# Kernel optimization log

Measured on AMD Instinct MI355X. Metric: run time of the kernel, lower is better.

Reference implementation:

```python
import jax, jax.numpy as jnp
import numpy as np

DN = ('NHWC', 'HWIO', 'NHWC')

def _conv1x1(x, k):
    # 1x1 conv, stride 1, SAME padding (channels_last)
    return jax.lax.conv_general_dilated(x, k, window_strides=(1, 1), padding='SAME', dimension_numbers=DN)

def setup_inputs() -> dict:
    key = jax.random.key(0)
    k1, k2, k3, k4, k5 = jax.random.split(key, 5)
    B, H, W, C = 4, 64, 64, 256
    c8 = C // 8
    x = jax.random.normal(k1, (B, H, W, C), dtype=jnp.float32)
    # Glorot-like scaling for stability
    kernel_f = jax.random.normal(k2, (1, 1, C, c8), dtype=jnp.float32) * (1.0 / np.sqrt(C))
    kernel_g = jax.random.normal(k3, (1, 1, C, c8), dtype=jnp.float32) * (1.0 / np.sqrt(C))
    kernel_h = jax.random.normal(k4, (1, 1, C, C), dtype=jnp.float32) * (1.0 / np.sqrt(C))
    gamma = jax.random.normal(k5, (), dtype=jnp.float32) * 0.1
    return {'x': x, 'kernel_f': kernel_f, 'kernel_g': kernel_g, 'kernel_h': kernel_h, 'gamma': gamma}

def reference(x, kernel_f, kernel_g, kernel_h, gamma):
    B, H, W, C = x.shape
    N = H * W
    f = _conv1x1(x, kernel_f).reshape(B, N, -1)   # [B, N, C/8] queries
    g = _conv1x1(x, kernel_g).reshape(B, N, -1)   # [B, N, C/8] keys
    h = _conv1x1(x, kernel_h).reshape(B, N, -1)   # [B, N, C]   values
    e = jnp.einsum('bnc,bmc->bnm', f, g)          # [B, N, N] scores
    attn = jax.nn.softmax(e, axis=-1)
    o = jnp.einsum('bnm,bmc->bnc', attn, h).reshape(B, H, W, C)
    return x + gamma * o
```

## Files before the change

### kernel.cpp

```cpp
#include <hip/hip_runtime.h>

typedef __attribute__((ext_vector_type(8))) short bf16x8;
typedef __attribute__((ext_vector_type(4))) float f32x4;
typedef __attribute__((ext_vector_type(16))) float f32x16;

__device__ __forceinline__ unsigned short f2bf(float f) {
    union { float f; unsigned u; } v; v.f = f;
    return (unsigned short)((v.u + 0x7FFFu + ((v.u >> 16) & 1u)) >> 16);
}

__device__ __forceinline__ float fexp2(float v) {
#if __has_builtin(__builtin_amdgcn_exp2f)
    return __builtin_amdgcn_exp2f(v);
#else
    float r; asm("v_exp_f32 %0, %1" : "=v"(r) : "v"(v)); return r;
#endif
}
__device__ __forceinline__ unsigned cvt_pk_bf16(float lo, float hi) {
    unsigned r;
    asm("v_cvt_pk_bf16_f32 %0, %1, %2" : "=v"(r) : "v"(lo), "v"(hi));
    return r;
}

__device__ __forceinline__ void async16(unsigned short* lds, const unsigned short* gsrc) {
    __builtin_amdgcn_global_load_lds(
        (const __attribute__((address_space(1))) void*)gsrc,
        (__attribute__((address_space(3))) void*)lds, 16, 0, 0);
}

__global__ __launch_bounds__(256) void k_wt(const float* __restrict__ kf,
                                            const float* __restrict__ kg,
                                            const float* __restrict__ kh,
                                            unsigned short* __restrict__ wt) {
    int n = blockIdx.x, t = threadIdx.x;
    const float* src; int stride, col;
    if (n < 32)      { src = kf; stride = 32;  col = n; }
    else if (n < 64) { src = kg; stride = 32;  col = n - 32; }
    else             { src = kh; stride = 256; col = n - 64; }
    float v = src[t * stride + col];
    if (n < 32) v *= 1.44269504088896341f;
    wt[n * 256 + (((t >> 3) ^ (n & 7)) << 3) + (t & 7)] = f2bf(v);
}

__global__ __launch_bounds__(512) void k_proj(const float* __restrict__ x,
                                              const unsigned short* __restrict__ wt,
                                              unsigned short* __restrict__ f,
                                              unsigned short* __restrict__ g,
                                              unsigned short* __restrict__ hT) {
    __shared__ unsigned short xs[8192];
    __shared__ unsigned short ws[16384];
    int t = threadIdx.x, rb = blockIdx.x;
    int w = t >> 6, lane = t & 63, q = lane >> 4, n15 = lane & 15;
    int b = rb >> 7, nbase = (rb & 127) * 32;
    int rg0 = w & 1, cg0 = w >> 1;
    int cgh = w & 3, rgh = w >> 2;

#pragma unroll
    for (int i = 0; i < 4; ++i) {
        int lin = i * 512 + t, row = lin >> 6, c4 = lin & 63;
        float4 v = *(const float4*)&x[(rb * 32 + row) * 256 + c4 * 4];
        ushort4 o; o.x = f2bf(v.x); o.y = f2bf(v.y); o.z = f2bf(v.z); o.w = f2bf(v.w);
        *(ushort4*)&xs[row * 256 + (((c4 >> 1) ^ (row & 7)) << 3) + ((c4 & 1) << 2)] = o;
    }
#pragma unroll
    for (int j = 0; j < 4; ++j)
        async16(&ws[(j * 512 + w * 64) * 8], wt + (j * 512 + t) * 8);
    __syncthreads();

    for (int ct = 0; ct < 5; ++ct) {
        f32x4 acc = (f32x4){0.f, 0.f, 0.f, 0.f};
        if (ct == 0) {
#pragma unroll
            for (int kk = 0; kk < 8; ++kk) {
                bf16x8 a = *(const bf16x8*)&xs[(rg0 * 16 + n15) * 256
                                + ((((kk << 2) + q) ^ (n15 & 7)) << 3)];
                bf16x8 bw = *(const bf16x8*)&ws[(cg0 * 16 + n15) * 256
                                + ((((kk << 2) + q) ^ (n15 & 7)) << 3)];
                acc = __builtin_amdgcn_mfma_f32_16x16x32_bf16(a, bw, acc, 0, 0, 0);
            }
        } else {
#pragma unroll
            for (int kk = 0; kk < 8; ++kk) {
                bf16x8 a = *(const bf16x8*)&ws[(cgh * 16 + n15) * 256
                                + ((((kk << 2) + q) ^ (n15 & 7)) << 3)];
                bf16x8 bx = *(const bf16x8*)&xs[(rgh * 16 + n15) * 256
                                + ((((kk << 2) + q) ^ (n15 & 7)) << 3)];
                acc = __builtin_amdgcn_mfma_f32_16x16x32_bf16(a, bx, acc, 0, 0, 0);
            }
        }
        __syncthreads();
        if (ct < 4) {
            const unsigned short* wsrc = wt + (ct + 1) * 16384;
#pragma unroll
            for (int j = 0; j < 4; ++j)
                async16(&ws[(j * 512 + w * 64) * 8], wsrc + (j * 512 + t) * 8);
        }
        if (ct == 0) {
#pragma unroll
            for (int r = 0; r < 4; ++r) {
                int grow = rb * 32 + rg0 * 16 + q * 4 + r;
                int col = cg0 * 16 + n15;
                unsigned short v = f2bf(acc[r]);
                if (col < 32) f[grow * 32 + col] = v;
                else          g[grow * 32 + (col - 32)] = v;
            }
        } else {
#pragma unroll
            for (int r = 0; r < 4; ++r) {
                int ch = (ct - 1) * 64 + cgh * 16 + q * 4 + r;
                int key = nbase + rgh * 16 + n15;
                hT[((b * 512 + (key >> 3)) * 256 + ch) * 8 + (key & 7)] = f2bf(acc[r]);
            }
        }
        __syncthreads();
    }
}

__global__ __launch_bounds__(512, 4) void k_attn(const float* __restrict__ x,
                                                 const unsigned short* __restrict__ f,
                                                 const unsigned short* __restrict__ g,
                                                 const unsigned short* __restrict__ hT,
                                                 const float* __restrict__ gamma_p,
                                                 float* __restrict__ out) {
    __shared__ unsigned short pls[2][4096];
    __shared__ float lpart[4][64];
    __shared__ __align__(16) float lrec[64];
    int t = threadIdx.x, bx = blockIdx.x;
    int b = (bx >> 1) & 3;
    int ch2 = (bx >> 3) & 1;
    int qt = ((bx & 1) << 5) | (bx >> 4);
    int qbase = qt * 64;
    int chbase = ch2 * 128;
    int w = t >> 6, l = t & 63;
    int hi = l >> 5, l31 = l & 31;
    int q = l >> 4, n15 = l & 15;
    int cb = w & 3;
    const bool is_s = (w < 4);

    bf16x8 aFB[4];
    const unsigned short* gW = g + (b * 4096 + w * 16 + n15) * 32 + q * 8;
    if (is_s) {
#pragma unroll
        for (int nt = 0; nt < 4; ++nt)
            aFB[nt] = *(const bf16x8*)&f[(b * 4096 + qbase + nt * 16 + n15) * 32 + q * 8];
    }
    bf16x8 aG, aGn;
    f32x4 lac = (f32x4){0.f, 0.f, 0.f, 0.f};
    const f32x4 zero4 = (f32x4){0.f, 0.f, 0.f, 0.f};

    const unsigned short* hb2 = hT + b * 1048576
                              + (chbase + cb * 32 + l31) * 8 + hi * 2048;
    bf16x8 bHc[4], bHn[4];

    auto s_tile = [&](int buf) {
        f32x4 sa[4];
#pragma unroll
        for (int nt = 0; nt < 4; ++nt)
            sa[nt] = __builtin_amdgcn_mfma_f32_16x16x32_bf16(aG, aFB[nt], zero4, 0, 0, 0);
        int kq = w * 4 + q;
#pragma unroll
        for (int nt = 0; nt < 4; ++nt) {
#pragma unroll
            for (int r = 0; r < 4; ++r) {
                sa[nt][r] = fexp2(sa[nt][r]);
                lac[nt] += sa[nt][r];
            }
            unsigned p0 = cvt_pk_bf16(sa[nt][0], sa[nt][1]);
            unsigned p1 = cvt_pk_bf16(sa[nt][2], sa[nt][3]);
            int row = nt * 16 + n15;
            unsigned* dst = (unsigned*)&pls[buf][row * 64]
                          + (((kq >> 1) ^ (n15 & 7)) << 2) + ((kq & 1) << 1);
            dst[0] = p0; dst[1] = p1;
        }
    };

    f32x16 o0, o1;
#pragma unroll
    for (int i = 0; i < 16; ++i) { o0[i] = 0.f; o1[i] = 0.f; }

    if (is_s) {
        aG  = *(const bf16x8*)&gW[0];
        aGn = *(const bf16x8*)&gW[2048];
        s_tile(0);
        aG = aGn;
        __builtin_amdgcn_sched_barrier(0);
        asm volatile("s_waitcnt lgkmcnt(0)" ::: "memory");
    } else {
#pragma unroll
        for (int ks = 0; ks < 4; ++ks)
            bHc[ks] = *(const bf16x8*)&hb2[ks * 4096];
        __builtin_amdgcn_sched_barrier(0);
    }
    __builtin_amdgcn_s_barrier();
    __builtin_amdgcn_sched_barrier(0);

#pragma unroll 2
    for (int kt = 0; kt < 64; ++kt) {
        int cur = kt & 1, nxt = cur ^ 1;

        if (is_s) {
            if (kt + 1 < 64) {
                int ktn = (kt + 2 < 64) ? kt + 2 : 63;
                aGn = *(const bf16x8*)&gW[ktn * 2048];
                s_tile(nxt);
                aG = aGn;
            }
            __builtin_amdgcn_sched_barrier(0);
            asm volatile("s_waitcnt lgkmcnt(0)" ::: "memory");
        } else {
            if (kt + 1 < 64) {
#pragma unroll
                for (int ks = 0; ks < 4; ++ks)
                    bHn[ks] = *(const bf16x8*)&hb2[(kt + 1) * 16384 + ks * 4096];
            }
            const unsigned short* pcur = &pls[cur][0];
            __builtin_amdgcn_s_setprio(1);
#pragma unroll
            for (int ks = 0; ks < 4; ++ks) {
                int seg = (((2 * ks + hi) ^ (l31 & 7)) << 3);
                bf16x8 aP0 = *(const bf16x8*)&pcur[l31 * 64 + seg];
                bf16x8 aP1 = *(const bf16x8*)&pcur[(32 + l31) * 64 + seg];
                o0 = __builtin_amdgcn_mfma_f32_32x32x16_bf16(aP0, bHc[ks], o0, 0, 0, 0);
                o1 = __builtin_amdgcn_mfma_f32_32x32x16_bf16(aP1, bHc[ks], o1, 0, 0, 0);
            }
            __builtin_amdgcn_s_setprio(0);
            if (kt + 1 < 64) {
#pragma unroll
                for (int ks = 0; ks < 4; ++ks) bHc[ks] = bHn[ks];
            }
            __builtin_amdgcn_sched_barrier(0);
        }

        __builtin_amdgcn_s_barrier();
        __builtin_amdgcn_sched_barrier(0);
    }

    if (is_s) {
#pragma unroll
        for (int nt = 0; nt < 4; ++nt) {
            float ps = lac[nt];
            ps += __shfl_xor(ps, 16);
            ps += __shfl_xor(ps, 32);
            if (q == 0) lpart[w][nt * 16 + n15] = ps;
        }
    }
    __syncthreads();
    if (t < 64) lrec[t] = 1.0f / (lpart[0][t] + lpart[1][t] + lpart[2][t] + lpart[3][t]);
    __syncthreads();
    if (!is_s) {
        float gam = *gamma_p;
        int ch = chbase + cb * 32 + l31;
#pragma unroll
        for (int qq = 0; qq < 4; ++qq) {
            int r0 = 8 * qq + 4 * hi;
            f32x4 ri0 = *(const f32x4*)&lrec[r0];
            f32x4 ri1 = *(const f32x4*)&lrec[32 + r0];
#pragma unroll
            for (int j = 0; j < 4; ++j) {
                int idx0 = (b * 4096 + qbase + r0 + j) * 256 + ch;
                int idx1 = idx0 + 32 * 256;
                out[idx0] = x[idx0] + gam * (o0[4 * qq + j] * ri0[j]);
                out[idx1] = x[idx1] + gam * (o1[4 * qq + j] * ri1[j]);
            }
        }
    }
}

extern "C" void kernel_launch(void* const* d_in, const int* in_sizes, int n_in,
                              void* d_out, int out_size, void* d_ws, size_t ws_size,
                              hipStream_t stream) {
    const float* x  = (const float*)d_in[0];
    const float* kf = (const float*)d_in[1];
    const float* kg = (const float*)d_in[2];
    const float* kh = (const float*)d_in[3];
    const float* gm = (const float*)d_in[4];
    float* out = (float*)d_out;

    char* ws = (char*)d_ws;
    unsigned short* wt = (unsigned short*)(ws);
    unsigned short* fb = (unsigned short*)(ws + 163840);
    unsigned short* gb = (unsigned short*)(ws + 1212416);
    unsigned short* hT = (unsigned short*)(ws + 2260992);

    hipLaunchKernelGGL(k_wt,   dim3(320), dim3(256), 0, stream, kf, kg, kh, wt);
    hipLaunchKernelGGL(k_proj, dim3(512), dim3(512), 0, stream, x, wt, fb, gb, hT);
    hipLaunchKernelGGL(k_attn, dim3(512), dim3(512), 0, stream, x, fb, gb, hT, gm, out);
}
```

Baseline: 136.6 us.

## Process two key tiles per barrier with quad-buffered P in LDS

The attention main loop now handles two 64-key tiles per iteration, using four LDS buffers for the exponentiated score tile P instead of two. This halves the number of block-wide barriers. Score warps issue two independent MFMA groups back to back, and PV warps run two tiles of MFMAs per phase with register double-buffered H loads. The cost is more LDS per block, which may lower occupancy under launch_bounds(512,4), and more registers.

Result: no change. 138.9 us (+1.7%).

```diff
diff --git a/kernel.cpp b/kernel.cpp
--- a/kernel.cpp
+++ b/kernel.cpp
@@ -122,7 +122,7 @@
                                                  const unsigned short* __restrict__ hT,
                                                  const float* __restrict__ gamma_p,
                                                  float* __restrict__ out) {
-    __shared__ unsigned short pls[2][4096];
+    __shared__ unsigned short pls[4][4096];
     __shared__ float lpart[4][64];
     __shared__ __align__(16) float lrec[64];
     int t = threadIdx.x, bx = blockIdx.x;
@@ -144,7 +144,6 @@
         for (int nt = 0; nt < 4; ++nt)
             aFB[nt] = *(const bf16x8*)&f[(b * 4096 + qbase + nt * 16 + n15) * 32 + q * 8];
     }
-    bf16x8 aG, aGn;
     f32x4 lac = (f32x4){0.f, 0.f, 0.f, 0.f};
     const f32x4 zero4 = (f32x4){0.f, 0.f, 0.f, 0.f};
 
@@ -152,11 +151,12 @@
                               + (chbase + cb * 32 + l31) * 8 + hi * 2048;
     bf16x8 bHc[4], bHn[4];
 
-    auto s_tile = [&](int buf) {
-        f32x4 sa[4];
+    auto s_mfma = [&](const bf16x8& aG, f32x4* sa) {
 #pragma unroll
         for (int nt = 0; nt < 4; ++nt)
             sa[nt] = __builtin_amdgcn_mfma_f32_16x16x32_bf16(aG, aFB[nt], zero4, 0, 0, 0);
+    };
+    auto s_finish = [&](f32x4* sa, int buf) {
         int kq = w * 4 + q;
 #pragma unroll
         for (int nt = 0; nt < 4; ++nt) {
@@ -178,11 +178,18 @@
 #pragma unroll
     for (int i = 0; i < 16; ++i) { o0[i] = 0.f; o1[i] = 0.f; }
 
+    bf16x8 aGa, aGb;
+
     if (is_s) {
-        aG  = *(const bf16x8*)&gW[0];
-        aGn = *(const bf16x8*)&gW[2048];
-        s_tile(0);
-        aG = aGn;
+        bf16x8 g0 = *(const bf16x8*)&gW[0];
+        bf16x8 g1 = *(const bf16x8*)&gW[2048];
+        f32x4 sa[4], sb[4];
+        s_mfma(g0, sa);
+        s_mfma(g1, sb);
+        aGa = *(const bf16x8*)&gW[2 * 2048];
+        aGb = *(const bf16x8*)&gW[3 * 2048];
+        s_finish(sa, 0);
+        s_finish(sb, 1);
         __builtin_amdgcn_sched_barrier(0);
         asm volatile("s_waitcnt lgkmcnt(0)" ::: "memory");
     } else {
@@ -194,40 +201,55 @@
     __builtin_amdgcn_s_barrier();
     __builtin_amdgcn_sched_barrier(0);
 
-#pragma unroll 2
-    for (int kt = 0; kt < 64; ++kt) {
-        int cur = kt & 1, nxt = cur ^ 1;
+    for (int p = 0; p < 32; ++p) {
+        int t0 = 2 * p, t1 = t0 + 1;
 
         if (is_s) {
-            if (kt + 1 < 64) {
-                int ktn = (kt + 2 < 64) ? kt + 2 : 63;
-                aGn = *(const bf16x8*)&gW[ktn * 2048];
-                s_tile(nxt);
-                aG = aGn;
+            if (p < 31) {
+                f32x4 sa[4], sb[4];
+                s_mfma(aGa, sa);
+                s_mfma(aGb, sb);
+                int ta = (t0 + 4 < 64) ? t0 + 4 : 63;
+                int tb = (t1 + 4 < 64) ? t1 + 4 : 63;
+                bf16x8 an = *(const bf16x8*)&gW[ta * 2048];
+                bf16x8 bn = *(const bf16x8*)&gW[tb * 2048];
+                s_finish(sa, (t0 + 2) & 3);
+                s_finish(sb, (t1 + 2) & 3);
+                aGa = an; aGb = bn;
             }
             __builtin_amdgcn_sched_barrier(0);
             asm volatile("s_waitcnt lgkmcnt(0)" ::: "memory");
         } else {
-            if (kt + 1 < 64) {
-#pragma unroll
-                for (int ks = 0; ks < 4; ++ks)
-                    bHn[ks] = *(const bf16x8*)&hb2[(kt + 1) * 16384 + ks * 4096];
-            }
-            const unsigned short* pcur = &pls[cur][0];
+#pragma unroll
+            for (int ks = 0; ks < 4; ++ks)
+                bHn[ks] = *(const bf16x8*)&hb2[t1 * 16384 + ks * 4096];
+            const unsigned short* pc0 = &pls[t0 & 3][0];
             __builtin_amdgcn_s_setprio(1);
 #pragma unroll
             for (int ks = 0; ks < 4; ++ks) {
                 int seg = (((2 * ks + hi) ^ (l31 & 7)) << 3);
-                bf16x8 aP0 = *(const bf16x8*)&pcur[l31 * 64 + seg];
-                bf16x8 aP1 = *(const bf16x8*)&pcur[(32 + l31) * 64 + seg];
+                bf16x8 aP0 = *(const bf16x8*)&pc0[l31 * 64 + seg];
+                bf16x8 aP1 = *(const bf16x8*)&pc0[(32 + l31) * 64 + seg];
                 o0 = __builtin_amdgcn_mfma_f32_32x32x16_bf16(aP0, bHc[ks], o0, 0, 0, 0);
                 o1 = __builtin_amdgcn_mfma_f32_32x32x16_bf16(aP1, bHc[ks], o1, 0, 0, 0);
             }
             __builtin_amdgcn_s_setprio(0);
-            if (kt + 1 < 64) {
-#pragma unroll
-                for (int ks = 0; ks < 4; ++ks) bHc[ks] = bHn[ks];
-            }
+            if (p < 31) {
+#pragma unroll
+                for (int ks = 0; ks < 4; ++ks)
+                    bHc[ks] = *(const bf16x8*)&hb2[(t0 + 2) * 16384 + ks * 4096];
+            }
+            const unsigned short* pc1 = &pls[t1 & 3][0];
+            __builtin_amdgcn_s_setprio(1);
+#pragma unroll
+            for (int ks = 0; ks < 4; ++ks) {
+                int seg = (((2 * ks + hi) ^ (l31 & 7)) << 3);
+                bf16x8 aP0 = *(const bf16x8*)&pc1[l31 * 64 + seg];
+                bf16x8 aP1 = *(const bf16x8*)&pc1[(32 + l31) * 64 + seg];
+                o0 = __builtin_amdgcn_mfma_f32_32x32x16_bf16(aP0, bHn[ks], o0, 0, 0, 0);
+                o1 = __builtin_amdgcn_mfma_f32_32x32x16_bf16(aP1, bHn[ks], o1, 0, 0, 0);
+            }
+            __builtin_amdgcn_s_setprio(0);
             __builtin_amdgcn_sched_barrier(0);
         }
 
```
